# Kernel optimization log

Measured on AMD Instinct MI355X. Metric: run time of the kernel, lower is better.

The kernel has to match this reference:

```python
import jax, jax.numpy as jnp
import numpy as np

N_VAR = 50000
N_CON = 50000
N_NODES = N_VAR + N_CON
N_EDGES = 800000
DIM = 64


def _mlp2(x, w1, b1, w2, b2):
    return jnp.maximum(x @ w1 + b1, 0.0) @ w2 + b2


def _edge_conv(x, edge_index, edge_types, w1, b1, w2, b2, num_nodes):
    # PyG MessagePassing flow 'source_to_target': x_j = x[src]=x[edge_index[0]],
    # x_i = x[dst]=x[edge_index[1]]; aggregate mean at dst.
    src, dst = edge_index[0], edge_index[1]
    feats = jnp.concatenate([x[dst], x[src], edge_types], axis=1)  # [E, 2*dim+2]
    msg = _mlp2(feats, w1, b1, w2, b2)                             # [E, dim]
    s = jax.ops.segment_sum(msg, dst, num_segments=num_nodes)
    cnt = jax.ops.segment_sum(jnp.ones((dst.shape[0], 1), msg.dtype), dst,
                              num_segments=num_nodes)
    return s / jnp.maximum(cnt, 1.0)


def setup_inputs() -> dict:
    key = jax.random.key(0)
    ks = jax.random.split(key, 32)

    def w(k, shape, fan_in):
        return jax.random.normal(k, shape, dtype=jnp.float32) * (1.0 / np.sqrt(fan_in))

    inp = {}
    inp['var_node_features'] = jax.random.normal(ks[0], (N_VAR, 2), dtype=jnp.float32)
    inp['con_node_features'] = jax.random.normal(ks[1], (N_CON, 2), dtype=jnp.float32)
    src = jax.random.randint(ks[2], (N_EDGES,), 0, N_NODES)
    dst = jax.random.randint(ks[3], (N_EDGES,), 0, N_NODES)
    inp['edge_index'] = jnp.stack([src, dst]).astype(jnp.int32)
    inp['edge_types'] = jax.random.normal(ks[4], (N_EDGES, 2), dtype=jnp.float32)
    inp['assoc_var'] = jnp.arange(N_VAR, dtype=jnp.int32)
    inp['assoc_con'] = jnp.arange(N_CON, dtype=jnp.int32) + N_VAR
    inp['num_nodes'] = N_NODES

    ki = 5
    for pre in ['var', 'con']:
        inp[f'{pre}_w1'] = w(ks[ki], (2, DIM), 2); ki += 1
        inp[f'{pre}_b1'] = jnp.zeros((DIM,), jnp.float32)
        inp[f'{pre}_w2'] = w(ks[ki], (DIM, DIM), DIM); ki += 1
        inp[f'{pre}_b2'] = jnp.zeros((DIM,), jnp.float32)
    for c in ['conv1', 'conv2', 'conv3']:
        inp[f'{c}_w1'] = w(ks[ki], (2 * DIM + 2, DIM), 2 * DIM + 2); ki += 1
        inp[f'{c}_b1'] = jnp.zeros((DIM,), jnp.float32)
        inp[f'{c}_w2'] = w(ks[ki], (DIM, DIM), DIM); ki += 1
        inp[f'{c}_b2'] = jnp.zeros((DIM,), jnp.float32)
    inp['fc1_w'] = w(ks[ki], (4 * DIM, DIM), 4 * DIM); ki += 1
    inp['fc1_b'] = jnp.zeros((DIM,), jnp.float32)
    inp['fc2_w'] = w(ks[ki], (DIM, DIM), DIM); ki += 1
    inp['fc2_b'] = jnp.zeros((DIM,), jnp.float32)
    inp['fc3_w'] = w(ks[ki], (DIM, 1), DIM); ki += 1
    inp['fc3_b'] = jnp.zeros((1,), jnp.float32)
    return inp


def reference(var_node_features, con_node_features, edge_types,
              var_w1, var_b1, var_w2, var_b2,
              con_w1, con_b1, con_w2, con_b2,
              conv1_w1, conv1_b1, conv1_w2, conv1_b2,
              conv2_w1, conv2_b1, conv2_w2, conv2_b2,
              conv3_w1, conv3_b1, conv3_w2, conv3_b2,
              fc1_w, fc1_b, fc2_w, fc2_b, fc3_w, fc3_b,
              edge_index, assoc_var, assoc_con, num_nodes):
    n = _mlp2(var_node_features, var_w1, var_b1, var_w2, var_b2)  # [n_var, dim]
    e = _mlp2(con_node_features, con_w1, con_b1, con_w2, con_b2)  # [n_con, dim]
    x = jnp.zeros((num_nodes, n.shape[-1]), dtype=n.dtype)
    x = x.at[assoc_var].set(n)
    x = x.at[assoc_con].set(e)
    xs = [x]
    xs.append(jnp.maximum(_edge_conv(xs[-1], edge_index, edge_types,
                                     conv1_w1, conv1_b1, conv1_w2, conv1_b2, num_nodes), 0.0))
    xs.append(jnp.maximum(_edge_conv(xs[-1], edge_index, edge_types,
                                     conv2_w1, conv2_b1, conv2_w2, conv2_b2, num_nodes), 0.0))
    xs.append(jnp.maximum(_edge_conv(xs[-1], edge_index, edge_types,
                                     conv3_w1, conv3_b1, conv3_w2, conv3_b2, num_nodes), 0.0))
    h = jnp.concatenate(xs, axis=-1)[assoc_var]          # [n_var, 4*dim]
    h = jnp.maximum(h @ fc1_w + fc1_b, 0.0)
    h = jnp.maximum(h @ fc2_w + fc2_b, 0.0)
    out = jax.nn.sigmoid(h @ fc3_w + fc3_b)
    return out.squeeze(-1)
```

## Files before the change

### kernel.cpp

```cpp
#include <hip/hip_runtime.h>
#include <hip/hip_bf16.h>
#include <math.h>


#define N_VARN 50000
#define NNODES 100000
#define NEDGES 800000
#define NB_SCAN 196

typedef __hip_bfloat16 bf16;

__device__ __forceinline__ float b2f(unsigned short u) {
  union { unsigned v; float f; } x;
  x.v = ((unsigned)u) << 16;
  return x.f;
}

__global__ __launch_bounds__(256) void embed_kernel(
    const float* __restrict__ vf, const float* __restrict__ cf,
    const float* __restrict__ vw1, const float* __restrict__ vb1,
    const float* __restrict__ vw2, const float* __restrict__ vb2,
    const float* __restrict__ cw1, const float* __restrict__ cb1,
    const float* __restrict__ cw2, const float* __restrict__ cb2,
    const int* __restrict__ av, const int* __restrict__ ac,
    const float* __restrict__ nw1, const float* __restrict__ nb1,
    bf16* __restrict__ x0, bf16* __restrict__ A16, bf16* __restrict__ B16) {
  __shared__ float sh[40][64];
  int tid = threadIdx.x, wid = tid >> 6, lane = tid & 63;
  int nodebase = blockIdx.x * 40;
  bool con = (nodebase >= N_VARN);
  const float* in = con ? cf : vf;
  const float* w1 = con ? cw1 : vw1;
  const float* b1 = con ? cb1 : vb1;
  const float* w2 = con ? cw2 : vw2;
  const float* b2 = con ? cb2 : vb2;
  const int* assoc = con ? ac : av;
  int ibase = con ? (nodebase - N_VARN) : nodebase;
  float w1a = w1[lane], w1b = w1[64 + lane], b1v = b1[lane];
  int n0 = wid * 10;
  int rows[10];
#pragma unroll 1
  for (int j = 0; j < 10; ++j) {
    int ni = ibase + n0 + j;
    rows[j] = assoc[ni];
    float i0 = in[ni * 2], i1 = in[ni * 2 + 1];
    sh[n0 + j][lane] = fmaxf(fmaf(i0, w1a, fmaf(i1, w1b, b1v)), 0.f);
  }
  float acc[10];
  float b2v = b2[lane];
#pragma unroll
  for (int j = 0; j < 10; ++j) acc[j] = b2v;
#pragma unroll 2
  for (int k4 = 0; k4 < 16; ++k4) {
    float w0 = w2[(k4 * 4 + 0) * 64 + lane];
    float w1v = w2[(k4 * 4 + 1) * 64 + lane];
    float w2v = w2[(k4 * 4 + 2) * 64 + lane];
    float w3v = w2[(k4 * 4 + 3) * 64 + lane];
#pragma unroll
    for (int j = 0; j < 10; ++j) {
      float4 hv = *(const float4*)&sh[n0 + j][k4 * 4];
      acc[j] = fmaf(hv.x, w0, acc[j]);
      acc[j] = fmaf(hv.y, w1v, acc[j]);
      acc[j] = fmaf(hv.z, w2v, acc[j]);
      acc[j] = fmaf(hv.w, w3v, acc[j]);
    }
  }
#pragma unroll
  for (int j = 0; j < 10; ++j) {
    x0[(size_t)rows[j] * 64 + lane] = __float2bfloat16(acc[j]);
    sh[n0 + j][lane] = acc[j];
  }
  float aa[10], bb[10];
  float nb1v = nb1[lane];
#pragma unroll
  for (int j = 0; j < 10; ++j) {
    aa[j] = nb1v;
    bb[j] = 0.f;
  }
#pragma unroll 2
  for (int k4 = 0; k4 < 16; ++k4) {
    float wa0 = nw1[(k4 * 4 + 0) * 64 + lane];
    float wa1 = nw1[(k4 * 4 + 1) * 64 + lane];
    float wa2 = nw1[(k4 * 4 + 2) * 64 + lane];
    float wa3 = nw1[(k4 * 4 + 3) * 64 + lane];
    float wb0 = nw1[(64 + k4 * 4 + 0) * 64 + lane];
    float wb1 = nw1[(64 + k4 * 4 + 1) * 64 + lane];
    float wb2 = nw1[(64 + k4 * 4 + 2) * 64 + lane];
    float wb3 = nw1[(64 + k4 * 4 + 3) * 64 + lane];
#pragma unroll
    for (int j = 0; j < 10; ++j) {
      float4 xv = *(const float4*)&sh[n0 + j][k4 * 4];
      aa[j] = fmaf(xv.x, wa0, aa[j]);
      aa[j] = fmaf(xv.y, wa1, aa[j]);
      aa[j] = fmaf(xv.z, wa2, aa[j]);
      aa[j] = fmaf(xv.w, wa3, aa[j]);
      bb[j] = fmaf(xv.x, wb0, bb[j]);
      bb[j] = fmaf(xv.y, wb1, bb[j]);
      bb[j] = fmaf(xv.z, wb2, bb[j]);
      bb[j] = fmaf(xv.w, wb3, bb[j]);
    }
  }
#pragma unroll
  for (int j = 0; j < 10; ++j) {
    A16[(size_t)rows[j] * 64 + lane] = __float2bfloat16(aa[j]);
    B16[(size_t)rows[j] * 64 + lane] = __float2bfloat16(bb[j]);
  }
}

__global__ __launch_bounds__(256) void hist_kernel(const int* __restrict__ ei,
                                                   unsigned* __restrict__ deg) {
  int e = blockIdx.x * 256 + threadIdx.x;
  atomicAdd(&deg[ei[NEDGES + e]], 1u);
}

__global__ __launch_bounds__(512) void scan1_kernel(
    const unsigned* __restrict__ deg, unsigned* __restrict__ blocksum) {
  __shared__ unsigned sm[512];
  int t = threadIdx.x;
  int i = blockIdx.x * 512 + t;
  sm[t] = (i < NNODES) ? deg[i] : 0u;
  __syncthreads();
  for (int off = 256; off > 0; off >>= 1) {
    if (t < off) sm[t] += sm[t + off];
    __syncthreads();
  }
  if (t == 0) blocksum[blockIdx.x] = sm[0];
}

__global__ __launch_bounds__(256) void scan2_kernel(
    const unsigned* __restrict__ blocksum, unsigned* __restrict__ blockoff) {
  __shared__ unsigned sm[256];
  int t = threadIdx.x;
  sm[t] = (t < NB_SCAN) ? blocksum[t] : 0u;
  __syncthreads();
  if (t == 0) {
    unsigned run = 0;
    for (int j = 0; j < NB_SCAN; ++j) {
      unsigned v = sm[j];
      sm[j] = run;
      run += v;
    }
  }
  __syncthreads();
  if (t < NB_SCAN) blockoff[t] = sm[t];
}

__global__ __launch_bounds__(512) void scan3_kernel(
    const unsigned* __restrict__ deg, const unsigned* __restrict__ blockoff,
    unsigned* __restrict__ rowptr) {
  __shared__ unsigned sm[512];
  int t = threadIdx.x;
  int i = blockIdx.x * 512 + t;
  unsigned v = (i < NNODES) ? deg[i] : 0u;
  sm[t] = v;
  __syncthreads();
  for (int off = 1; off < 512; off <<= 1) {
    unsigned add = (t >= off) ? sm[t - off] : 0u;
    __syncthreads();
    sm[t] += add;
    __syncthreads();
  }
  if (i <= NNODES) rowptr[i] = blockoff[blockIdx.x] + sm[t] - v;
}

__global__ __launch_bounds__(256) void scatter_kernel(
    const int* __restrict__ ei, const float* __restrict__ et,
    const unsigned* __restrict__ rowptr, unsigned* __restrict__ cursor,
    int4* __restrict__ erec) {
  int e = blockIdx.x * 256 + threadIdx.x;
  int d = ei[NEDGES + e];
  float2 t = ((const float2*)et)[e];
  unsigned pos = rowptr[d] + atomicAdd(&cursor[d], 1u);
  int4 r;
  r.x = ei[e];
  r.y = __float_as_int(t.x);
  r.z = __float_as_int(t.y);
  r.w = 0;
  erec[pos] = r;
}

#define AG_NPW 5
template <bool FUSE>
__global__ __launch_bounds__(512) void agg_kernel(
    const unsigned* __restrict__ rowptr, const int4* __restrict__ erec,
    const bf16* __restrict__ A16i, const bf16* __restrict__ B16i,
    const float* __restrict__ w1c, const float* __restrict__ w2,
    const float* __restrict__ b2, bf16* __restrict__ xout,
    const float* __restrict__ nw1, const float* __restrict__ nb1,
    bf16* __restrict__ A16o, bf16* __restrict__ B16o) {
  __shared__ float sh[40][64];
  __shared__ float shc[40];
  int tid = threadIdx.x, wid = tid >> 6, lane = tid & 63;
  int half = lane >> 5;
  int fl = lane & 31;
  int nodebase = blockIdx.x * 40;
  int n0 = wid * AG_NPW;
  float2 c0p = *(const float2*)&w1c[fl * 2];
  float2 c1p = *(const float2*)&w1c[64 + fl * 2];
#pragma unroll 1
  for (int j = 0; j < AG_NPW; ++j) {
    int node = nodebase + n0 + j;
    unsigned beg = rowptr[node], end = rowptr[node + 1];
    ushort2 au = *(const ushort2*)((const unsigned short*)A16i +
                                   (size_t)node * 64 + fl * 2);
    float ax = b2f(au.x), ay = b2f(au.y);
    float accx0 = 0.f, accy0 = 0.f, accx1 = 0.f, accy1 = 0.f;
    float accx2 = 0.f, accy2 = 0.f, accx3 = 0.f, accy3 = 0.f;
    unsigned i = beg;
    for (; i + 8 <= end; i += 8) {
      int4 r0 = erec[i + half];
      int4 r1 = erec[i + 2 + half];
      int4 r2 = erec[i + 4 + half];
      int4 r3 = erec[i + 6 + half];
      ushort2 b0 = *(const ushort2*)((const unsigned short*)B16i +
                                     (size_t)r0.x * 64 + fl * 2);
      ushort2 b1 = *(const ushort2*)((const unsigned short*)B16i +
                                     (size_t)r1.x * 64 + fl * 2);
      ushort2 b2u = *(const ushort2*)((const unsigned short*)B16i +
                                      (size_t)r2.x * 64 + fl * 2);
      ushort2 b3 = *(const ushort2*)((const unsigned short*)B16i +
                                     (size_t)r3.x * 64 + fl * 2);
      float t0x = __int_as_float(r0.y), t0y = __int_as_float(r0.z);
      float t1x = __int_as_float(r1.y), t1y = __int_as_float(r1.z);
      float t2x = __int_as_float(r2.y), t2y = __int_as_float(r2.z);
      float t3x = __int_as_float(r3.y), t3y = __int_as_float(r3.z);
      accx0 += fmaxf(ax + b2f(b0.x) + fmaf(t0x, c0p.x, t0y * c1p.x), 0.f);
      accy0 += fmaxf(ay + b2f(b0.y) + fmaf(t0x, c0p.y, t0y * c1p.y), 0.f);
      accx1 += fmaxf(ax + b2f(b1.x) + fmaf(t1x, c0p.x, t1y * c1p.x), 0.f);
      accy1 += fmaxf(ay + b2f(b1.y) + fmaf(t1x, c0p.y, t1y * c1p.y), 0.f);
      accx2 += fmaxf(ax + b2f(b2u.x) + fmaf(t2x, c0p.x, t2y * c1p.x), 0.f);
      accy2 += fmaxf(ay + b2f(b2u.y) + fmaf(t2x, c0p.y, t2y * c1p.y), 0.f);
      accx3 += fmaxf(ax + b2f(b3.x) + fmaf(t3x, c0p.x, t3y * c1p.x), 0.f);
      accy3 += fmaxf(ay + b2f(b3.y) + fmaf(t3x, c0p.y, t3y * c1p.y), 0.f);
    }
    for (; i + 4 <= end; i += 4) {
      int4 r0 = erec[i + half];
      int4 r1 = erec[i + 2 + half];
      ushort2 b0 = *(const ushort2*)((const unsigned short*)B16i +
                                     (size_t)r0.x * 64 + fl * 2);
      ushort2 b1 = *(const ushort2*)((const unsigned short*)B16i +
                                     (size_t)r1.x * 64 + fl * 2);
      float t0x = __int_as_float(r0.y), t0y = __int_as_float(r0.z);
      float t1x = __int_as_float(r1.y), t1y = __int_as_float(r1.z);
      accx0 += fmaxf(ax + b2f(b0.x) + fmaf(t0x, c0p.x, t0y * c1p.x), 0.f);
      accy0 += fmaxf(ay + b2f(b0.y) + fmaf(t0x, c0p.y, t0y * c1p.y), 0.f);
      accx1 += fmaxf(ax + b2f(b1.x) + fmaf(t1x, c0p.x, t1y * c1p.x), 0.f);
      accy1 += fmaxf(ay + b2f(b1.y) + fmaf(t1x, c0p.y, t1y * c1p.y), 0.f);
    }
    for (; i < end; i += 2) {
      if (i + half < end) {
        int4 r = erec[i + half];
        float tx = __int_as_float(r.y), ty = __int_as_float(r.z);
        ushort2 bu = *(const ushort2*)((const unsigned short*)B16i +
                                       (size_t)r.x * 64 + fl * 2);
        accx0 += fmaxf(ax + b2f(bu.x) + fmaf(tx, c0p.x, ty * c1p.x), 0.f);
        accy0 += fmaxf(ay + b2f(bu.y) + fmaf(tx, c0p.y, ty * c1p.y), 0.f);
      }
    }
    float accx = (accx0 + accx1) + (accx2 + accx3);
    float accy = (accy0 + accy1) + (accy2 + accy3);
    accx += __shfl_xor(accx, 32);
    accy += __shfl_xor(accy, 32);
    if (half == 0) *(float2*)&sh[n0 + j][fl * 2] = make_float2(accx, accy);
    if (lane == 0) shc[n0 + j] = (float)(end - beg);
  }
  float o[AG_NPW];
  float b2l = b2[lane];
#pragma unroll
  for (int j = 0; j < AG_NPW; ++j) o[j] = shc[n0 + j] * b2l;
#pragma unroll 2
  for (int k4 = 0; k4 < 16; ++k4) {
    float w0 = w2[(k4 * 4 + 0) * 64 + lane];
    float w1v = w2[(k4 * 4 + 1) * 64 + lane];
    float w2v = w2[(k4 * 4 + 2) * 64 + lane];
    float w3v = w2[(k4 * 4 + 3) * 64 + lane];
#pragma unroll
    for (int j = 0; j < AG_NPW; ++j) {
      float4 sv = *(const float4*)&sh[n0 + j][k4 * 4];
      o[j] = fmaf(sv.x, w0, o[j]);
      o[j] = fmaf(sv.y, w1v, o[j]);
      o[j] = fmaf(sv.z, w2v, o[j]);
      o[j] = fmaf(sv.w, w3v, o[j]);
    }
  }
#pragma unroll
  for (int j = 0; j < AG_NPW; ++j) {
    float cn = shc[n0 + j];
    float r = fmaxf(o[j] / fmaxf(cn, 1.f), 0.f);
    o[j] = r;
    xout[(size_t)(nodebase + n0 + j) * 64 + lane] = __float2bfloat16(r);
  }
  if (FUSE) {
#pragma unroll
    for (int j = 0; j < AG_NPW; ++j) sh[n0 + j][lane] = o[j];
    float aa[AG_NPW], bb[AG_NPW];
    float nb1v = nb1[lane];
#pragma unroll
    for (int j = 0; j < AG_NPW; ++j) {
      aa[j] = nb1v;
      bb[j] = 0.f;
    }
#pragma unroll 2
    for (int k4 = 0; k4 < 16; ++k4) {
      float wa0 = nw1[(k4 * 4 + 0) * 64 + lane];
      float wa1 = nw1[(k4 * 4 + 1) * 64 + lane];
      float wa2 = nw1[(k4 * 4 + 2) * 64 + lane];
      float wa3 = nw1[(k4 * 4 + 3) * 64 + lane];
      float wb0 = nw1[(64 + k4 * 4 + 0) * 64 + lane];
      float wb1 = nw1[(64 + k4 * 4 + 1) * 64 + lane];
      float wb2 = nw1[(64 + k4 * 4 + 2) * 64 + lane];
      float wb3 = nw1[(64 + k4 * 4 + 3) * 64 + lane];
#pragma unroll
      for (int j = 0; j < AG_NPW; ++j) {
        float4 xv = *(const float4*)&sh[n0 + j][k4 * 4];
        aa[j] = fmaf(xv.x, wa0, aa[j]);
        aa[j] = fmaf(xv.y, wa1, aa[j]);
        aa[j] = fmaf(xv.z, wa2, aa[j]);
        aa[j] = fmaf(xv.w, wa3, aa[j]);
        bb[j] = fmaf(xv.x, wb0, bb[j]);
        bb[j] = fmaf(xv.y, wb1, bb[j]);
        bb[j] = fmaf(xv.z, wb2, bb[j]);
        bb[j] = fmaf(xv.w, wb3, bb[j]);
      }
    }
#pragma unroll
    for (int j = 0; j < AG_NPW; ++j) {
      A16o[(size_t)(nodebase + n0 + j) * 64 + lane] = __float2bfloat16(aa[j]);
      B16o[(size_t)(nodebase + n0 + j) * 64 + lane] = __float2bfloat16(bb[j]);
    }
  }
}

#define HB_NODES 40
#define HB_NPW 5
__global__ __launch_bounds__(512) void head_kernel(
    const bf16* __restrict__ x0, const bf16* __restrict__ x1,
    const bf16* __restrict__ x2, const bf16* __restrict__ x3,
    const int* __restrict__ av,
    const float* __restrict__ fc1w, const float* __restrict__ fc1b,
    const float* __restrict__ fc2w, const float* __restrict__ fc2b,
    const float* __restrict__ fc3w, const float* __restrict__ fc3b,
    float* __restrict__ out) {
  __shared__ float h[HB_NODES][256];
  int tid = threadIdx.x;
  int nodebase = blockIdx.x * HB_NODES;
  for (int idx = tid; idx < HB_NODES * 16; idx += 512) {
    int n = idx >> 4, c4 = idx & 15;
    int row = av[nodebase + n];
    const unsigned short* p0 = (const unsigned short*)x0 + (size_t)row * 64;
    const unsigned short* p1 = (const unsigned short*)x1 + (size_t)row * 64;
    const unsigned short* p2 = (const unsigned short*)x2 + (size_t)row * 64;
    const unsigned short* p3 = (const unsigned short*)x3 + (size_t)row * 64;
    ushort4 u0 = *(const ushort4*)(p0 + c4 * 4);
    ushort4 u1 = *(const ushort4*)(p1 + c4 * 4);
    ushort4 u2 = *(const ushort4*)(p2 + c4 * 4);
    ushort4 u3 = *(const ushort4*)(p3 + c4 * 4);
    float* dstp = &h[n][0];
    *(float4*)(dstp + c4 * 4) =
        make_float4(b2f(u0.x), b2f(u0.y), b2f(u0.z), b2f(u0.w));
    *(float4*)(dstp + 64 + c4 * 4) =
        make_float4(b2f(u1.x), b2f(u1.y), b2f(u1.z), b2f(u1.w));
    *(float4*)(dstp + 128 + c4 * 4) =
        make_float4(b2f(u2.x), b2f(u2.y), b2f(u2.z), b2f(u2.w));
    *(float4*)(dstp + 192 + c4 * 4) =
        make_float4(b2f(u3.x), b2f(u3.y), b2f(u3.z), b2f(u3.w));
  }
  __syncthreads();
  int wid = tid >> 6, lane = tid & 63;
  int n0 = wid * HB_NPW;
  float acc[HB_NPW];
#pragma unroll
  for (int j = 0; j < HB_NPW; ++j) acc[j] = fc1b[lane];
#pragma unroll 2
  for (int k4 = 0; k4 < 64; ++k4) {
    float w0 = fc1w[(k4 * 4 + 0) * 64 + lane];
    float w1v = fc1w[(k4 * 4 + 1) * 64 + lane];
    float w2v = fc1w[(k4 * 4 + 2) * 64 + lane];
    float w3v = fc1w[(k4 * 4 + 3) * 64 + lane];
#pragma unroll
    for (int j = 0; j < HB_NPW; ++j) {
      float4 hv = *(const float4*)&h[n0 + j][k4 * 4];
      acc[j] = fmaf(hv.x, w0, acc[j]);
      acc[j] = fmaf(hv.y, w1v, acc[j]);
      acc[j] = fmaf(hv.z, w2v, acc[j]);
      acc[j] = fmaf(hv.w, w3v, acc[j]);
    }
  }
  __syncthreads();
  float* h2 = &h[0][0];
#pragma unroll
  for (int j = 0; j < HB_NPW; ++j) h2[(n0 + j) * 64 + lane] = fmaxf(acc[j], 0.f);
  __syncthreads();
  float acc2[HB_NPW];
#pragma unroll
  for (int j = 0; j < HB_NPW; ++j) acc2[j] = fc2b[lane];
#pragma unroll 2
  for (int k4 = 0; k4 < 16; ++k4) {
    float w0 = fc2w[(k4 * 4 + 0) * 64 + lane];
    float w1v = fc2w[(k4 * 4 + 1) * 64 + lane];
    float w2v = fc2w[(k4 * 4 + 2) * 64 + lane];
    float w3v = fc2w[(k4 * 4 + 3) * 64 + lane];
#pragma unroll
    for (int j = 0; j < HB_NPW; ++j) {
      float4 hv = *(const float4*)&h2[(n0 + j) * 64 + k4 * 4];
      acc2[j] = fmaf(hv.x, w0, acc2[j]);
      acc2[j] = fmaf(hv.y, w1v, acc2[j]);
      acc2[j] = fmaf(hv.z, w2v, acc2[j]);
      acc2[j] = fmaf(hv.w, w3v, acc2[j]);
    }
  }
  float w3l = fc3w[lane];
  float b3 = fc3b[0];
#pragma unroll
  for (int j = 0; j < HB_NPW; ++j) {
    float p = fmaxf(acc2[j], 0.f) * w3l;
#pragma unroll
    for (int off = 32; off; off >>= 1) p += __shfl_xor(p, off);
    if (lane == j) out[nodebase + n0 + j] = 1.f / (1.f + expf(-(p + b3)));
  }
}

extern "C" void kernel_launch(void* const* d_in, const int* in_sizes, int n_in,
                              void* d_out, int out_size, void* d_ws,
                              size_t ws_size, hipStream_t stream) {
  const float* vf = (const float*)d_in[0];
  const float* cf = (const float*)d_in[1];
  const int* ei = (const int*)d_in[2];
  const float* et = (const float*)d_in[3];
  const int* av = (const int*)d_in[4];
  const int* ac = (const int*)d_in[5];
  const float* vw1 = (const float*)d_in[7];
  const float* vb1 = (const float*)d_in[8];
  const float* vw2 = (const float*)d_in[9];
  const float* vb2 = (const float*)d_in[10];
  const float* cw1 = (const float*)d_in[11];
  const float* cb1 = (const float*)d_in[12];
  const float* cw2 = (const float*)d_in[13];
  const float* cb2 = (const float*)d_in[14];
  const float* convw1[3] = {(const float*)d_in[15], (const float*)d_in[19],
                            (const float*)d_in[23]};
  const float* convb1[3] = {(const float*)d_in[16], (const float*)d_in[20],
                            (const float*)d_in[24]};
  const float* convw2[3] = {(const float*)d_in[17], (const float*)d_in[21],
                            (const float*)d_in[25]};
  const float* convb2[3] = {(const float*)d_in[18], (const float*)d_in[22],
                            (const float*)d_in[26]};
  const float* fc1w = (const float*)d_in[27];
  const float* fc1b = (const float*)d_in[28];
  const float* fc2w = (const float*)d_in[29];
  const float* fc2b = (const float*)d_in[30];
  const float* fc3w = (const float*)d_in[31];
  const float* fc3b = (const float*)d_in[32];

  char* wsb = (char*)d_ws;
  const size_t ROWB16 = (size_t)NNODES * 64 * sizeof(bf16);
  bf16* x[4];
  x[0] = (bf16*)(wsb);
  x[1] = (bf16*)(wsb + ROWB16);
  x[2] = (bf16*)(wsb + 2 * ROWB16);
  x[3] = (bf16*)(wsb + 3 * ROWB16);
  bf16* A16 = (bf16*)(wsb + 4 * ROWB16);
  bf16* B16 = (bf16*)(wsb + 5 * ROWB16);
  bf16* A16b = (bf16*)(wsb + 6 * ROWB16);
  bf16* B16b = (bf16*)(wsb + 7 * ROWB16);
  int4* erec = (int4*)(wsb + 8 * ROWB16);
  unsigned* rowptr = (unsigned*)((char*)erec + (size_t)NEDGES * 16);
  unsigned* deg = rowptr + NNODES + 1;
  unsigned* cursor = deg + NNODES;
  unsigned* blocksum = cursor + NNODES;
  unsigned* blockoff = blocksum + 256;

  embed_kernel<<<NNODES / 40, 256, 0, stream>>>(
      vf, cf, vw1, vb1, vw2, vb2, cw1, cb1, cw2, cb2, av, ac, convw1[0],
      convb1[0], x[0], A16, B16);

  hipMemsetAsync(deg, 0, 2 * NNODES * sizeof(unsigned), stream);
  hist_kernel<<<NEDGES / 256, 256, 0, stream>>>(ei, deg);
  scan1_kernel<<<NB_SCAN, 512, 0, stream>>>(deg, blocksum);
  scan2_kernel<<<1, 256, 0, stream>>>(blocksum, blockoff);
  scan3_kernel<<<NB_SCAN, 512, 0, stream>>>(deg, blockoff, rowptr);
  scatter_kernel<<<NEDGES / 256, 256, 0, stream>>>(ei, et, rowptr, cursor,
                                                   erec);

  agg_kernel<true><<<NNODES / 40, 512, 0, stream>>>(
      rowptr, erec, A16, B16, convw1[0] + 128 * 64, convw2[0], convb2[0],
      x[1], convw1[1], convb1[1], A16b, B16b);
  agg_kernel<true><<<NNODES / 40, 512, 0, stream>>>(
      rowptr, erec, A16b, B16b, convw1[1] + 128 * 64, convw2[1], convb2[1],
      x[2], convw1[2], convb1[2], A16, B16);
  agg_kernel<false><<<N_VARN / 40, 512, 0, stream>>>(
      rowptr, erec, A16, B16, convw1[2] + 128 * 64, convw2[2], convb2[2],
      x[3], nullptr, nullptr, nullptr, nullptr);

  head_kernel<<<N_VARN / HB_NODES, 512, 0, stream>>>(
      x[0], x[1], x[2], x[3], av, fc1w, fc1b, fc2w, fc2b, fc3w, fc3b,
      (float*)d_out);
}
```

Before: 541.3 us.

## Widen agg gathers to 4 edges per wave and skip unused con x0 writes

The aggregation kernel now splits each wavefront into four 16-lane groups. Each lane loads four bf16 features (8 bytes) per gathered neighbor row, so a wave processes 4 edges per step instead of 2, with wider loads and fewer tail iterations; the partial sums are reduced with two xor shuffles. The embed kernel moves to 512 threads with 5 nodes per wave, and it skips writing x0 for constraint nodes, since only variable rows of x0 are read later by the head. The wider grouping aims to raise memory-level parallelism in the gather, at the cost of more shuffles and possible idle lanes for low-degree nodes.

```diff
diff --git a/kernel.cpp b/kernel.cpp
--- a/kernel.cpp
+++ b/kernel.cpp
@@ -16,7 +16,7 @@
   return x.f;
 }
 
-__global__ __launch_bounds__(256) void embed_kernel(
+__global__ __launch_bounds__(512) void embed_kernel(
     const float* __restrict__ vf, const float* __restrict__ cf,
     const float* __restrict__ vw1, const float* __restrict__ vb1,
     const float* __restrict__ vw2, const float* __restrict__ vb2,
@@ -37,19 +37,19 @@
   const int* assoc = con ? ac : av;
   int ibase = con ? (nodebase - N_VARN) : nodebase;
   float w1a = w1[lane], w1b = w1[64 + lane], b1v = b1[lane];
-  int n0 = wid * 10;
-  int rows[10];
+  int n0 = wid * 5;
+  int rows[5];
 #pragma unroll 1
-  for (int j = 0; j < 10; ++j) {
+  for (int j = 0; j < 5; ++j) {
     int ni = ibase + n0 + j;
     rows[j] = assoc[ni];
     float i0 = in[ni * 2], i1 = in[ni * 2 + 1];
     sh[n0 + j][lane] = fmaxf(fmaf(i0, w1a, fmaf(i1, w1b, b1v)), 0.f);
   }
-  float acc[10];
+  float acc[5];
   float b2v = b2[lane];
 #pragma unroll
-  for (int j = 0; j < 10; ++j) acc[j] = b2v;
+  for (int j = 0; j < 5; ++j) acc[j] = b2v;
 #pragma unroll 2
   for (int k4 = 0; k4 < 16; ++k4) {
     float w0 = w2[(k4 * 4 + 0) * 64 + lane];
@@ -57,7 +57,7 @@
     float w2v = w2[(k4 * 4 + 2) * 64 + lane];
     float w3v = w2[(k4 * 4 + 3) * 64 + lane];
 #pragma unroll
-    for (int j = 0; j < 10; ++j) {
+    for (int j = 0; j < 5; ++j) {
       float4 hv = *(const float4*)&sh[n0 + j][k4 * 4];
       acc[j] = fmaf(hv.x, w0, acc[j]);
       acc[j] = fmaf(hv.y, w1v, acc[j]);
@@ -66,14 +66,14 @@
     }
   }
 #pragma unroll
-  for (int j = 0; j < 10; ++j) {
-    x0[(size_t)rows[j] * 64 + lane] = __float2bfloat16(acc[j]);
+  for (int j = 0; j < 5; ++j) {
+    if (!con) x0[(size_t)rows[j] * 64 + lane] = __float2bfloat16(acc[j]);
     sh[n0 + j][lane] = acc[j];
   }
-  float aa[10], bb[10];
+  float aa[5], bb[5];
   float nb1v = nb1[lane];
 #pragma unroll
-  for (int j = 0; j < 10; ++j) {
+  for (int j = 0; j < 5; ++j) {
     aa[j] = nb1v;
     bb[j] = 0.f;
   }
@@ -88,7 +88,7 @@
     float wb2 = nw1[(64 + k4 * 4 + 2) * 64 + lane];
     float wb3 = nw1[(64 + k4 * 4 + 3) * 64 + lane];
 #pragma unroll
-    for (int j = 0; j < 10; ++j) {
+    for (int j = 0; j < 5; ++j) {
       float4 xv = *(const float4*)&sh[n0 + j][k4 * 4];
       aa[j] = fmaf(xv.x, wa0, aa[j]);
       aa[j] = fmaf(xv.y, wa1, aa[j]);
@@ -101,7 +101,7 @@
     }
   }
 #pragma unroll
-  for (int j = 0; j < 10; ++j) {
+  for (int j = 0; j < 5; ++j) {
     A16[(size_t)rows[j] * 64 + lane] = __float2bfloat16(aa[j]);
     B16[(size_t)rows[j] * 64 + lane] = __float2bfloat16(bb[j]);
   }
@@ -191,77 +191,62 @@
   __shared__ float sh[40][64];
   __shared__ float shc[40];
   int tid = threadIdx.x, wid = tid >> 6, lane = tid & 63;
-  int half = lane >> 5;
-  int fl = lane & 31;
+  int q = lane >> 4;
+  int fq = lane & 15;
   int nodebase = blockIdx.x * 40;
   int n0 = wid * AG_NPW;
-  float2 c0p = *(const float2*)&w1c[fl * 2];
-  float2 c1p = *(const float2*)&w1c[64 + fl * 2];
+  float4 c0q = *(const float4*)&w1c[fq * 4];
+  float4 c1q = *(const float4*)&w1c[64 + fq * 4];
 #pragma unroll 1
   for (int j = 0; j < AG_NPW; ++j) {
     int node = nodebase + n0 + j;
     unsigned beg = rowptr[node], end = rowptr[node + 1];
-    ushort2 au = *(const ushort2*)((const unsigned short*)A16i +
-                                   (size_t)node * 64 + fl * 2);
-    float ax = b2f(au.x), ay = b2f(au.y);
-    float accx0 = 0.f, accy0 = 0.f, accx1 = 0.f, accy1 = 0.f;
-    float accx2 = 0.f, accy2 = 0.f, accx3 = 0.f, accy3 = 0.f;
+    ushort4 au = *(const ushort4*)((const unsigned short*)A16i +
+                                   (size_t)node * 64 + fq * 4);
+    float a0 = b2f(au.x), a1 = b2f(au.y), a2 = b2f(au.z), a3 = b2f(au.w);
+    float4 accA = make_float4(0.f, 0.f, 0.f, 0.f);
+    float4 accB = make_float4(0.f, 0.f, 0.f, 0.f);
     unsigned i = beg;
     for (; i + 8 <= end; i += 8) {
-      int4 r0 = erec[i + half];
-      int4 r1 = erec[i + 2 + half];
-      int4 r2 = erec[i + 4 + half];
-      int4 r3 = erec[i + 6 + half];
-      ushort2 b0 = *(const ushort2*)((const unsigned short*)B16i +
-                                     (size_t)r0.x * 64 + fl * 2);
-      ushort2 b1 = *(const ushort2*)((const unsigned short*)B16i +
-                                     (size_t)r1.x * 64 + fl * 2);
-      ushort2 b2u = *(const ushort2*)((const unsigned short*)B16i +
-                                      (size_t)r2.x * 64 + fl * 2);
-      ushort2 b3 = *(const ushort2*)((const unsigned short*)B16i +
-                                     (size_t)r3.x * 64 + fl * 2);
-      float t0x = __int_as_float(r0.y), t0y = __int_as_float(r0.z);
-      float t1x = __int_as_float(r1.y), t1y = __int_as_float(r1.z);
-      float t2x = __int_as_float(r2.y), t2y = __int_as_float(r2.z);
-      float t3x = __int_as_float(r3.y), t3y = __int_as_float(r3.z);
-      accx0 += fmaxf(ax + b2f(b0.x) + fmaf(t0x, c0p.x, t0y * c1p.x), 0.f);
-      accy0 += fmaxf(ay + b2f(b0.y) + fmaf(t0x, c0p.y, t0y * c1p.y), 0.f);
-      accx1 += fmaxf(ax + b2f(b1.x) + fmaf(t1x, c0p.x, t1y * c1p.x), 0.f);
-      accy1 += fmaxf(ay + b2f(b1.y) + fmaf(t1x, c0p.y, t1y * c1p.y), 0.f);
-      accx2 += fmaxf(ax + b2f(b2u.x) + fmaf(t2x, c0p.x, t2y * c1p.x), 0.f);
-      accy2 += fmaxf(ay + b2f(b2u.y) + fmaf(t2x, c0p.y, t2y * c1p.y), 0.f);
-      accx3 += fmaxf(ax + b2f(b3.x) + fmaf(t3x, c0p.x, t3y * c1p.x), 0.f);
-      accy3 += fmaxf(ay + b2f(b3.y) + fmaf(t3x, c0p.y, t3y * c1p.y), 0.f);
-    }
-    for (; i + 4 <= end; i += 4) {
-      int4 r0 = erec[i + half];
-      int4 r1 = erec[i + 2 + half];
-      ushort2 b0 = *(const ushort2*)((const unsigned short*)B16i +
-                                     (size_t)r0.x * 64 + fl * 2);
-      ushort2 b1 = *(const ushort2*)((const unsigned short*)B16i +
-                                     (size_t)r1.x * 64 + fl * 2);
-      float t0x = __int_as_float(r0.y), t0y = __int_as_float(r0.z);
-      float t1x = __int_as_float(r1.y), t1y = __int_as_float(r1.z);
-      accx0 += fmaxf(ax + b2f(b0.x) + fmaf(t0x, c0p.x, t0y * c1p.x), 0.f);
-      accy0 += fmaxf(ay + b2f(b0.y) + fmaf(t0x, c0p.y, t0y * c1p.y), 0.f);
-      accx1 += fmaxf(ax + b2f(b1.x) + fmaf(t1x, c0p.x, t1y * c1p.x), 0.f);
-      accy1 += fmaxf(ay + b2f(b1.y) + fmaf(t1x, c0p.y, t1y * c1p.y), 0.f);
-    }
-    for (; i < end; i += 2) {
-      if (i + half < end) {
-        int4 r = erec[i + half];
+      int4 rA = erec[i + q];
+      int4 rB = erec[i + 4 + q];
+      ushort4 bA = *(const ushort4*)((const unsigned short*)B16i +
+                                     (size_t)rA.x * 64 + fq * 4);
+      ushort4 bB = *(const ushort4*)((const unsigned short*)B16i +
+                                     (size_t)rB.x * 64 + fq * 4);
+      float tAx = __int_as_float(rA.y), tAy = __int_as_float(rA.z);
+      float tBx = __int_as_float(rB.y), tBy = __int_as_float(rB.z);
+      accA.x += fmaxf(a0 + b2f(bA.x) + fmaf(tAx, c0q.x, tAy * c1q.x), 0.f);
+      accA.y += fmaxf(a1 + b2f(bA.y) + fmaf(tAx, c0q.y, tAy * c1q.y), 0.f);
+      accA.z += fmaxf(a2 + b2f(bA.z) + fmaf(tAx, c0q.z, tAy * c1q.z), 0.f);
+      accA.w += fmaxf(a3 + b2f(bA.w) + fmaf(tAx, c0q.w, tAy * c1q.w), 0.f);
+      accB.x += fmaxf(a0 + b2f(bB.x) + fmaf(tBx, c0q.x, tBy * c1q.x), 0.f);
+      accB.y += fmaxf(a1 + b2f(bB.y) + fmaf(tBx, c0q.y, tBy * c1q.y), 0.f);
+      accB.z += fmaxf(a2 + b2f(bB.z) + fmaf(tBx, c0q.z, tBy * c1q.z), 0.f);
+      accB.w += fmaxf(a3 + b2f(bB.w) + fmaf(tBx, c0q.w, tBy * c1q.w), 0.f);
+    }
+    for (; i < end; i += 4) {
+      if (i + q < end) {
+        int4 r = erec[i + q];
+        ushort4 bu = *(const ushort4*)((const unsigned short*)B16i +
+                                       (size_t)r.x * 64 + fq * 4);
         float tx = __int_as_float(r.y), ty = __int_as_float(r.z);
-        ushort2 bu = *(const ushort2*)((const unsigned short*)B16i +
-                                       (size_t)r.x * 64 + fl * 2);
-        accx0 += fmaxf(ax + b2f(bu.x) + fmaf(tx, c0p.x, ty * c1p.x), 0.f);
-        accy0 += fmaxf(ay + b2f(bu.y) + fmaf(tx, c0p.y, ty * c1p.y), 0.f);
+        accA.x += fmaxf(a0 + b2f(bu.x) + fmaf(tx, c0q.x, ty * c1q.x), 0.f);
+        accA.y += fmaxf(a1 + b2f(bu.y) + fmaf(tx, c0q.y, ty * c1q.y), 0.f);
+        accA.z += fmaxf(a2 + b2f(bu.z) + fmaf(tx, c0q.z, ty * c1q.z), 0.f);
+        accA.w += fmaxf(a3 + b2f(bu.w) + fmaf(tx, c0q.w, ty * c1q.w), 0.f);
       }
     }
-    float accx = (accx0 + accx1) + (accx2 + accx3);
-    float accy = (accy0 + accy1) + (accy2 + accy3);
-    accx += __shfl_xor(accx, 32);
-    accy += __shfl_xor(accy, 32);
-    if (half == 0) *(float2*)&sh[n0 + j][fl * 2] = make_float2(accx, accy);
+    float4 acc;
+    acc.x = accA.x + accB.x;
+    acc.y = accA.y + accB.y;
+    acc.z = accA.z + accB.z;
+    acc.w = accA.w + accB.w;
+    acc.x += __shfl_xor(acc.x, 16); acc.x += __shfl_xor(acc.x, 32);
+    acc.y += __shfl_xor(acc.y, 16); acc.y += __shfl_xor(acc.y, 32);
+    acc.z += __shfl_xor(acc.z, 16); acc.z += __shfl_xor(acc.z, 32);
+    acc.w += __shfl_xor(acc.w, 16); acc.w += __shfl_xor(acc.w, 32);
+    if (lane < 16) *(float4*)&sh[n0 + j][fq * 4] = acc;
     if (lane == 0) shc[n0 + j] = (float)(end - beg);
   }
   float o[AG_NPW];
@@ -470,7 +455,7 @@
   unsigned* blocksum = cursor + NNODES;
   unsigned* blockoff = blocksum + 256;
 
-  embed_kernel<<<NNODES / 40, 256, 0, stream>>>(
+  embed_kernel<<<NNODES / 40, 512, 0, stream>>>(
       vf, cf, vw1, vb1, vw2, vb2, cw1, cb1, cw2, cb2, av, ac, convw1[0],
       convb1[0], x[0], A16, B16);
 
```

Measured after the change: 526.0 us. -2.8%, faster.
